# Kernel optimization log

Measured on AMD Instinct MI355X. Metric: run time of the kernel, lower is better.

The kernel has to match this reference:

```python
import jax, jax.numpy as jnp
import numpy as np

IN_FEATURES = 20000   # genes
OUT_FEATURES = 3000   # pathways
NNZ = 600000          # sparsity = 1 - NNZ/(IN*OUT) = 0.99
BATCH = 8192          # cells


def setup_inputs() -> dict:
    key = jax.random.key(0)
    k_w, k_b, k_x = jax.random.split(key, 3)

    # Unique, coalesced (sorted by row-major flat index) COO pattern, mimicking
    # torch_sparse.coalesce: sample with slight oversampling, dedupe, truncate.
    rng = np.random.default_rng(0)
    flat = np.unique(rng.integers(0, IN_FEATURES * OUT_FEATURES,
                                  size=NNZ + 20000, dtype=np.int64))[:NNZ]
    rows = jnp.asarray(flat // IN_FEATURES, dtype=jnp.int32)   # [nnz] in [0, OUT)
    cols = jnp.asarray(flat % IN_FEATURES, dtype=jnp.int32)    # [nnz] in [0, IN)

    stdv = 1.0 / np.sqrt(OUT_FEATURES)  # reset_parameters uses 1/sqrt(out_features)
    weights = jax.random.uniform(k_w, (NNZ,), minval=-stdv, maxval=stdv,
                                 dtype=jnp.float32)
    bias = jax.random.uniform(k_b, (OUT_FEATURES,), minval=-stdv, maxval=stdv,
                              dtype=jnp.float32)
    inputs = jax.random.normal(k_x, (BATCH, IN_FEATURES), dtype=jnp.float32)
    return {"inputs": inputs, "weights": weights, "bias": bias,
            "rows": rows, "cols": cols}


def reference(inputs, weights, bias, rows, cols):
    # y = x @ W^T + b, where W is the sparse [out, in] matrix defined by
    # (rows, cols, weights). Indices are unique (coalesced), so scatter-add
    # into a dense W reproduces torch_sparse.spmm exactly.
    out_features = bias.shape[0]
    in_features = inputs.shape[-1]
    W = jnp.zeros((out_features, in_features), dtype=inputs.dtype)
    W = W.at[rows, cols].add(weights)              # [out, in] dense view of sparse W
    return inputs @ W.T + bias                     # [batch, out]
```

## Files before the change

### kernel.cpp

```cpp
#include <hip/hip_runtime.h>
#include <stdint.h>

#define IN_F   20000
#define OUT_F  3000
#define BATCH  8192

__global__ __launch_bounds__(256)
void k_transpose(const float* __restrict__ x, uint16_t* __restrict__ xT) {
    __shared__ float tile[128][65];
    const int c0 = blockIdx.x * 64;
    const int b0 = blockIdx.y * 128;
    const int tid = threadIdx.x;

#pragma unroll
    for (int i = 0; i < 8; ++i) {
        int idx = tid + i * 256;
        int b = idx >> 4, cq = idx & 15;
        int cc = c0 + cq * 4;
        float4 v = make_float4(0.f, 0.f, 0.f, 0.f);
        if (cc < IN_F)
            v = *(const float4*)&x[(size_t)(b0 + b) * IN_F + cc];
        tile[b][cq * 4 + 0] = v.x;
        tile[b][cq * 4 + 1] = v.y;
        tile[b][cq * 4 + 2] = v.z;
        tile[b][cq * 4 + 3] = v.w;
    }
    __syncthreads();

#pragma unroll
    for (int i = 0; i < 16; ++i) {
        int idx = tid + i * 256;
        int c = idx >> 6, bp = idx & 63;
        int cc = c0 + c;
        if (cc < IN_F) {
            uint32_t u0 = __float_as_uint(tile[2 * bp + 0][c]);
            uint32_t u1 = __float_as_uint(tile[2 * bp + 1][c]);
            uint32_t r0 = (u0 + 0x7fffu + ((u0 >> 16) & 1u)) >> 16;
            uint32_t r1 = (u1 + 0x7fffu + ((u1 >> 16) & 1u)) >> 16;
            *(uint32_t*)&xT[(size_t)cc * BATCH + (b0 + 2 * bp)] = r0 | (r1 << 16);
        }
    }
}

__global__ __launch_bounds__(256)
void k_row_ptr(const int* __restrict__ rows, int* __restrict__ row_ptr, int nnz) {
    int k = blockIdx.x * 256 + threadIdx.x;
    if (k >= nnz) return;
    int r  = rows[k];
    int rp = (k == 0) ? -1 : rows[k - 1];
    for (int q = rp + 1; q <= r; ++q) row_ptr[q] = k;
    if (k == nnz - 1) {
        for (int q = r + 1; q <= OUT_F; ++q) row_ptr[q] = nnz;
    }
}

#define ROWS_PB 16
#define LANES   8
#define BT      128
#define NRG     ((OUT_F + ROWS_PB - 1) / ROWS_PB)
#define NTILES  (BATCH / BT)
#define TPX     (NTILES / 8)

#define BF_LO(u) __uint_as_float((u) << 16)
#define BF_HI(u) __uint_as_float((u) & 0xffff0000u)
#define FMA8(A, q, wv)                                              \
    A[0] = fmaf(wv, BF_LO((q).x), A[0]);                            \
    A[1] = fmaf(wv, BF_HI((q).x), A[1]);                            \
    A[2] = fmaf(wv, BF_LO((q).y), A[2]);                            \
    A[3] = fmaf(wv, BF_HI((q).y), A[3]);                            \
    A[4] = fmaf(wv, BF_LO((q).z), A[4]);                            \
    A[5] = fmaf(wv, BF_HI((q).z), A[5]);                            \
    A[6] = fmaf(wv, BF_LO((q).w), A[6]);                            \
    A[7] = fmaf(wv, BF_HI((q).w), A[7]);

__global__ __launch_bounds__(128)
void k_spmm(const uint16_t* __restrict__ xT, const float* __restrict__ w,
            const float* __restrict__ bias, const int* __restrict__ cols,
            const int* __restrict__ row_ptr, float* __restrict__ out) {
    const int i = blockIdx.x;
    const int xcd = i & 7;
    const int j = i >> 3;
    const int tile_local = j / NRG;
    const int row_grp   = j - tile_local * NRG;
    const int tile = xcd + 8 * tile_local;
    const int b0 = tile * BT;

    const int t = threadIdx.x;
    const int row_sub = t >> 3;
    const int lane8  = t & 7;
    const int r = row_grp * ROWS_PB + row_sub;
    if (r >= OUT_F) return;

    const int kbeg = row_ptr[r];
    const int kend = row_ptr[r + 1];

    const uint16_t* xbase = xT + (size_t)(b0 + lane8 * 16);

    float acc[16];
#pragma unroll
    for (int e = 0; e < 16; ++e) acc[e] = 0.f;

    int k = kbeg;
    for (; k + 1 < kend; k += 2) {
        int   c0 = cols[k],   c1 = cols[k + 1];
        float w0 = w[k],      w1 = w[k + 1];
        const uint16_t* a0 = xbase + ((size_t)c0 << 13);
        const uint16_t* a1 = xbase + ((size_t)c1 << 13);
        uint4 q0 = *(const uint4*)(a0);
        uint4 q1 = *(const uint4*)(a0 + 8);
        uint4 q2 = *(const uint4*)(a1);
        uint4 q3 = *(const uint4*)(a1 + 8);
        FMA8(acc,       q0, w0);
        FMA8((acc + 8), q1, w0);
        FMA8(acc,       q2, w1);
        FMA8((acc + 8), q3, w1);
    }
    if (k < kend) {
        int   c0 = cols[k];
        float w0 = w[k];
        const uint16_t* a0 = xbase + ((size_t)c0 << 13);
        uint4 q0 = *(const uint4*)(a0);
        uint4 q1 = *(const uint4*)(a0 + 8);
        FMA8(acc,       q0, w0);
        FMA8((acc + 8), q1, w0);
    }

    const float bv = bias[r];
    const int   bb = b0 + lane8 * 16;
#pragma unroll
    for (int e = 0; e < 16; ++e) {
        out[(size_t)(bb + e) * OUT_F + r] = acc[e] + bv;
    }
}

extern "C" void kernel_launch(void* const* d_in, const int* in_sizes, int n_in,
                              void* d_out, int out_size, void* d_ws, size_t ws_size,
                              hipStream_t stream) {
    const float* x    = (const float*)d_in[0];
    const float* w    = (const float*)d_in[1];
    const float* bias = (const float*)d_in[2];
    const int*   rows = (const int*)d_in[3];
    const int*   cols = (const int*)d_in[4];
    float*       out  = (float*)d_out;
    const int    nnz  = in_sizes[1];

    int*      row_ptr = (int*)d_ws;
    uint16_t* xT      = (uint16_t*)((char*)d_ws + 16384);

    dim3 gT((IN_F + 63) / 64, BATCH / 128);
    hipLaunchKernelGGL(k_transpose, gT, dim3(256), 0, stream, x, xT);
    hipLaunchKernelGGL(k_row_ptr, dim3((nnz + 255) / 256), dim3(256), 0, stream,
                       rows, row_ptr, nnz);
    hipLaunchKernelGGL(k_spmm, dim3(8 * TPX * NRG), dim3(128), 0, stream,
                       xT, w, bias, cols, row_ptr, out);
}
```

Baseline: 2.232 ms.

## Process batch in chunks, halve SpMM batch tile, software-pipeline index loads

The batch is split into four chunks, and each chunk gets its own transpose and SpMM launch. The xT slice for a chunk then stays small enough to be served from cache while the SpMM gathers from it. The SpMM batch tile drops from 128 to 64 with 8 accumulators per thread and occupancy hints, and the inner loop is unrolled by 4 with the next cols and weights prefetched. The transpose now rounds to bf16 before writing to shared memory, which halves the LDS footprint. The cost is more kernel launches and a row-stride xT layout that still indexes the full batch, so the cache footprint depends on the chunk's address range.

Measured after the change: 2.164 ms. -3.0%, faster.

```diff
diff --git a/kernel.cpp b/kernel.cpp
--- a/kernel.cpp
+++ b/kernel.cpp
@@ -5,11 +5,15 @@
 #define OUT_F  3000
 #define BATCH  8192
 
+#define CHUNK     2048
+#define NCHUNKS   (BATCH / CHUNK)
+
 __global__ __launch_bounds__(256)
-void k_transpose(const float* __restrict__ x, uint16_t* __restrict__ xT) {
-    __shared__ float tile[128][65];
+void k_transpose(const float* __restrict__ x, uint16_t* __restrict__ xT,
+                 int b_base) {
+    __shared__ uint16_t tile[128][68];
     const int c0 = blockIdx.x * 64;
-    const int b0 = blockIdx.y * 128;
+    const int b0 = b_base + blockIdx.y * 128;
     const int tid = threadIdx.x;
 
 #pragma unroll
@@ -20,10 +24,14 @@
         float4 v = make_float4(0.f, 0.f, 0.f, 0.f);
         if (cc < IN_F)
             v = *(const float4*)&x[(size_t)(b0 + b) * IN_F + cc];
-        tile[b][cq * 4 + 0] = v.x;
-        tile[b][cq * 4 + 1] = v.y;
-        tile[b][cq * 4 + 2] = v.z;
-        tile[b][cq * 4 + 3] = v.w;
+        uint32_t u0 = __float_as_uint(v.x), u1 = __float_as_uint(v.y);
+        uint32_t u2 = __float_as_uint(v.z), u3 = __float_as_uint(v.w);
+        uint32_t r0 = (u0 + 0x7fffu + ((u0 >> 16) & 1u)) >> 16;
+        uint32_t r1 = (u1 + 0x7fffu + ((u1 >> 16) & 1u)) >> 16;
+        uint32_t r2 = (u2 + 0x7fffu + ((u2 >> 16) & 1u)) >> 16;
+        uint32_t r3 = (u3 + 0x7fffu + ((u3 >> 16) & 1u)) >> 16;
+        uint2 pk = make_uint2(r0 | (r1 << 16), r2 | (r3 << 16));
+        *(uint2*)&tile[b][cq * 4] = pk;
     }
     __syncthreads();
 
@@ -33,11 +41,9 @@
         int c = idx >> 6, bp = idx & 63;
         int cc = c0 + c;
         if (cc < IN_F) {
-            uint32_t u0 = __float_as_uint(tile[2 * bp + 0][c]);
-            uint32_t u1 = __float_as_uint(tile[2 * bp + 1][c]);
-            uint32_t r0 = (u0 + 0x7fffu + ((u0 >> 16) & 1u)) >> 16;
-            uint32_t r1 = (u1 + 0x7fffu + ((u1 >> 16) & 1u)) >> 16;
-            *(uint32_t*)&xT[(size_t)cc * BATCH + (b0 + 2 * bp)] = r0 | (r1 << 16);
+            uint32_t lo = tile[2 * bp + 0][c];
+            uint32_t hi = tile[2 * bp + 1][c];
+            *(uint32_t*)&xT[(size_t)cc * BATCH + (b0 + 2 * bp)] = lo | (hi << 16);
         }
     }
 }
@@ -55,10 +61,9 @@
 }
 
 #define ROWS_PB 16
-#define LANES   8
-#define BT      128
+#define BT      64
 #define NRG     ((OUT_F + ROWS_PB - 1) / ROWS_PB)
-#define NTILES  (BATCH / BT)
+#define NTILES  (CHUNK / BT)
 #define TPX     (NTILES / 8)
 
 #define BF_LO(u) __uint_as_float((u) << 16)
@@ -73,17 +78,18 @@
     A[6] = fmaf(wv, BF_LO((q).w), A[6]);                            \
     A[7] = fmaf(wv, BF_HI((q).w), A[7]);
 
-__global__ __launch_bounds__(128)
+__global__ __launch_bounds__(128, 8)
 void k_spmm(const uint16_t* __restrict__ xT, const float* __restrict__ w,
             const float* __restrict__ bias, const int* __restrict__ cols,
-            const int* __restrict__ row_ptr, float* __restrict__ out) {
+            const int* __restrict__ row_ptr, float* __restrict__ out,
+            int b_base) {
     const int i = blockIdx.x;
     const int xcd = i & 7;
     const int j = i >> 3;
     const int tile_local = j / NRG;
     const int row_grp   = j - tile_local * NRG;
     const int tile = xcd + 8 * tile_local;
-    const int b0 = tile * BT;
+    const int b0 = b_base + tile * BT;
 
     const int t = threadIdx.x;
     const int row_sub = t >> 3;
@@ -94,41 +100,51 @@
     const int kbeg = row_ptr[r];
     const int kend = row_ptr[r + 1];
 
-    const uint16_t* xbase = xT + (size_t)(b0 + lane8 * 16);
+    const uint16_t* xbase = xT + (size_t)(b0 + lane8 * 8);
 
-    float acc[16];
+    float acc[8];
 #pragma unroll
-    for (int e = 0; e < 16; ++e) acc[e] = 0.f;
+    for (int e = 0; e < 8; ++e) acc[e] = 0.f;
 
     int k = kbeg;
-    for (; k + 1 < kend; k += 2) {
-        int   c0 = cols[k],   c1 = cols[k + 1];
-        float w0 = w[k],      w1 = w[k + 1];
-        const uint16_t* a0 = xbase + ((size_t)c0 << 13);
-        const uint16_t* a1 = xbase + ((size_t)c1 << 13);
-        uint4 q0 = *(const uint4*)(a0);
-        uint4 q1 = *(const uint4*)(a0 + 8);
-        uint4 q2 = *(const uint4*)(a1);
-        uint4 q3 = *(const uint4*)(a1 + 8);
-        FMA8(acc,       q0, w0);
-        FMA8((acc + 8), q1, w0);
-        FMA8(acc,       q2, w1);
-        FMA8((acc + 8), q3, w1);
+    int   c0n = 0, c1n = 0, c2n = 0, c3n = 0;
+    float w0n = 0.f, w1n = 0.f, w2n = 0.f, w3n = 0.f;
+    if (k + 3 < kend) {
+        c0n = cols[k];     c1n = cols[k + 1];
+        c2n = cols[k + 2]; c3n = cols[k + 3];
+        w0n = w[k];     w1n = w[k + 1];
+        w2n = w[k + 2]; w3n = w[k + 3];
     }
-    if (k < kend) {
-        int   c0 = cols[k];
-        float w0 = w[k];
-        const uint16_t* a0 = xbase + ((size_t)c0 << 13);
-        uint4 q0 = *(const uint4*)(a0);
-        uint4 q1 = *(const uint4*)(a0 + 8);
-        FMA8(acc,       q0, w0);
-        FMA8((acc + 8), q1, w0);
+    while (k + 3 < kend) {
+        const int   c0 = c0n, c1 = c1n, c2 = c2n, c3 = c3n;
+        const float w0 = w0n, w1 = w1n, w2 = w2n, w3 = w3n;
+        uint4 q0 = *(const uint4*)(xbase + ((size_t)c0 << 13));
+        uint4 q1 = *(const uint4*)(xbase + ((size_t)c1 << 13));
+        uint4 q2 = *(const uint4*)(xbase + ((size_t)c2 << 13));
+        uint4 q3 = *(const uint4*)(xbase + ((size_t)c3 << 13));
+        k += 4;
+        if (k + 3 < kend) {
+            c0n = cols[k];     c1n = cols[k + 1];
+            c2n = cols[k + 2]; c3n = cols[k + 3];
+            w0n = w[k];     w1n = w[k + 1];
+            w2n = w[k + 2]; w3n = w[k + 3];
+        }
+        FMA8(acc, q0, w0);
+        FMA8(acc, q1, w1);
+        FMA8(acc, q2, w2);
+        FMA8(acc, q3, w3);
+    }
+    for (; k < kend; ++k) {
+        int   c  = cols[k];
+        float wv = w[k];
+        uint4 q = *(const uint4*)(xbase + ((size_t)c << 13));
+        FMA8(acc, q, wv);
     }
 
     const float bv = bias[r];
-    const int   bb = b0 + lane8 * 16;
+    const int   bb = b0 + lane8 * 8;
 #pragma unroll
-    for (int e = 0; e < 16; ++e) {
+    for (int e = 0; e < 8; ++e) {
         out[(size_t)(bb + e) * OUT_F + r] = acc[e] + bv;
     }
 }
@@ -147,10 +163,14 @@
     int*      row_ptr = (int*)d_ws;
     uint16_t* xT      = (uint16_t*)((char*)d_ws + 16384);
 
-    dim3 gT((IN_F + 63) / 64, BATCH / 128);
-    hipLaunchKernelGGL(k_transpose, gT, dim3(256), 0, stream, x, xT);
     hipLaunchKernelGGL(k_row_ptr, dim3((nnz + 255) / 256), dim3(256), 0, stream,
                        rows, row_ptr, nnz);
-    hipLaunchKernelGGL(k_spmm, dim3(8 * TPX * NRG), dim3(128), 0, stream,
-                       xT, w, bias, cols, row_ptr, out);
+
+    dim3 gT((IN_F + 63) / 64, CHUNK / 128);
+    for (int ch = 0; ch < NCHUNKS; ++ch) {
+        int b_base = ch * CHUNK;
+        hipLaunchKernelGGL(k_transpose, gT, dim3(256), 0, stream, x, xT, b_base);
+        hipLaunchKernelGGL(k_spmm, dim3(8 * TPX * NRG), dim3(128), 0, stream,
+                           xT, w, bias, cols, row_ptr, out, b_base);
+    }
 }
```
